# Performance work log

Hardware: AMD Instinct MI355X
Metric: run time of the kernel (lower is better)

Reference implementation:

```python
import jax, jax.numpy as jnp
import numpy as np
from jax import lax

B, T, A, L, H, FD = 32, 64, 6, 32, 128, 256


def setup_inputs() -> dict:
    key = jax.random.key(0)
    ks = jax.random.split(key, 24)
    rn = lambda k, s, sc: jax.random.normal(k, s, jnp.float32) * sc
    return {
        "states": rn(ks[0], (B, T, 3, 64, 64), 1.0),
        "actions": rn(ks[1], (B, T, A), 1.0),
        # CNN encoder params (scale ~ 1/sqrt(fan_in))
        "c1_w": rn(ks[2], (32, 3, 4, 4), 0.14), "c1_b": rn(ks[3], (32,), 0.01),
        "c2_w": rn(ks[4], (64, 32, 4, 4), 0.044), "c2_b": rn(ks[5], (64,), 0.01),
        "c3_w": rn(ks[6], (128, 64, 4, 4), 0.031), "c3_b": rn(ks[7], (128,), 0.01),
        "c4_w": rn(ks[8], (256, 128, 4, 4), 0.022), "c4_b": rn(ks[9], (256,), 0.01),
        "fc_w": rn(ks[10], (FD, 256 * 4 * 4), 0.0156), "fc_b": rn(ks[11], (FD,), 0.01),
        # GRUCell params (torch layout: W_ih (3H, in), W_hh (3H, H))
        "gru_wih": rn(ks[12], (3 * H, L + A), 0.16), "gru_whh": rn(ks[13], (3 * H, H), 0.088),
        "gru_bih": rn(ks[14], (3 * H,), 0.01), "gru_bhh": rn(ks[15], (3 * H,), 0.01),
        "prior_w": rn(ks[16], (2 * L, H), 0.088), "prior_b": rn(ks[17], (2 * L,), 0.01),
        "post_w": rn(ks[18], (2 * L, H + FD), 0.05), "post_b": rn(ks[19], (2 * L,), 0.01),
        # reparameterization noise (randn_like in torch), one per (b, t)
        "eps": rn(ks[20], (B, T, L), 1.0),
    }


def _conv(x, w, b):
    # Conv2d(k=4, stride=2, pad=1), NCHW/OIHW
    y = lax.conv_general_dilated(x, w, window_strides=(2, 2),
                                 padding=[(1, 1), (1, 1)],
                                 dimension_numbers=("NCHW", "OIHW", "NCHW"))
    return jax.nn.relu(y + b[None, :, None, None])


def _encode(x, c1_w, c1_b, c2_w, c2_b, c3_w, c3_b, c4_w, c4_b, fc_w, fc_b):
    # x: (N, 3, 64, 64) -> (N, FD)
    x = _conv(x, c1_w, c1_b)
    x = _conv(x, c2_w, c2_b)
    x = _conv(x, c3_w, c3_b)
    x = _conv(x, c4_w, c4_b)  # (N, 256, 4, 4)
    x = x.reshape(x.shape[0], -1)
    return x @ fc_w.T + fc_b


def _gru_cell(x, h, wih, whh, bih, bhh):
    gi = x @ wih.T + bih
    gh = h @ whh.T + bhh
    i_r, i_z, i_n = jnp.split(gi, 3, axis=-1)
    h_r, h_z, h_n = jnp.split(gh, 3, axis=-1)
    r = jax.nn.sigmoid(i_r + h_r)
    z = jax.nn.sigmoid(i_z + h_z)
    n = jnp.tanh(i_n + r * h_n)
    return (1.0 - z) * n + z * h


def reference(states, actions, c1_w, c1_b, c2_w, c2_b, c3_w, c3_b, c4_w, c4_b,
              fc_w, fc_b, gru_wih, gru_whh, gru_bih, gru_bhh,
              prior_w, prior_b, post_w, post_b, eps):
    b, t = states.shape[0], states.shape[1]
    # encoder has no recurrent dependency: encode all frames at once
    feats = _encode(states.reshape(b * t, *states.shape[2:]),
                    c1_w, c1_b, c2_w, c2_b, c3_w, c3_b, c4_w, c4_b,
                    fc_w, fc_b).reshape(b, t, -1)  # (B, T, FD)

    def step(carry, inp):
        h, z = carry
        a_t, f_t, e_t = inp
        h = _gru_cell(jnp.concatenate([z, a_t], -1), h,
                      gru_wih, gru_whh, gru_bih, gru_bhh)
        mu_p, lv_p = jnp.split(h @ prior_w.T + prior_b, 2, axis=-1)
        mu_q, lv_q = jnp.split(jnp.concatenate([h, f_t], -1) @ post_w.T + post_b, 2, axis=-1)
        z = mu_q + jnp.exp(0.5 * lv_q) * e_t
        return (h, z), (mu_p, lv_p, mu_q, lv_q, h, z)

    h0 = jnp.zeros((b, gru_whh.shape[1]), states.dtype)
    z0 = jnp.zeros((b, prior_w.shape[0] // 2), states.dtype)
    xs = (jnp.swapaxes(actions, 0, 1), jnp.swapaxes(feats, 0, 1),
          jnp.swapaxes(eps, 0, 1))
    _, ys = lax.scan(step, (h0, z0), xs)
    # (T, B, d) -> (B, T, d)
    return tuple(jnp.swapaxes(y, 0, 1) for y in ys)
```

## Files before the change

### kernel.cpp

```cpp
#include <hip/hip_runtime.h>
#include <math.h>

#define Bn 32
#define Tn 64
#define An 6
#define Ln 32
#define Hn 128
#define FDn 256
#define Nimg (Bn*Tn)

typedef __attribute__((ext_vector_type(8))) short frag_ab;
typedef __attribute__((ext_vector_type(4))) float frag_cd;
typedef _Float16 h2_t __attribute__((ext_vector_type(2)));

__device__ __forceinline__ float sigmoid_fast(float x){
  return __builtin_amdgcn_rcpf(1.f + __expf(-x));
}
__device__ __forceinline__ float tanh_fast(float x){
  float x2 = fminf(fmaxf(2.f*x, -30.f), 30.f);
  float e = __expf(x2);
  return (e - 1.f) * __builtin_amdgcn_rcpf(e + 1.f);
}

__device__ __forceinline__ unsigned short f2bf(float f){
  unsigned int u = __float_as_uint(f);
  unsigned int r = (u + 0x7fffu + ((u >> 16) & 1u)) >> 16;
  return (unsigned short)r;
}
__device__ __forceinline__ unsigned packh(float a, float b){
  union { h2_t h; unsigned u; } x;
  x.h = (h2_t){(_Float16)a, (_Float16)b};
  return x.u;
}
__device__ __forceinline__ float fdot2u(unsigned a, unsigned b, float c){
  union { unsigned u; h2_t h; } ua, ub;
  ua.u = a; ub.u = b;
#if __has_builtin(__builtin_amdgcn_fdot2)
  return __builtin_amdgcn_fdot2(ua.h, ub.h, c, false);
#else
  return c + (float)ua.h.x*(float)ub.h.x + (float)ua.h.y*(float)ub.h.y;
#endif
}
#define BAR_LDS() asm volatile("s_waitcnt lgkmcnt(0)\n\ts_barrier" ::: "memory")

__device__ __forceinline__ int swz_w(int r, int p){
  return ((r >> 4) << 9) + (p << 7) + ((((r & 15) ^ (p << 2))) << 3);
}
__device__ __forceinline__ int swz_r(int f, int l){
  return (f << 9) + ((l >> 4) << 7) + ((((l & 15) ^ ((l >> 4) << 2))) << 3);
}

__global__ void __launch_bounds__(256)
states_nhwc_kernel(const float* __restrict__ src, unsigned short* __restrict__ dst)
{
  int idx = blockIdx.x*256 + threadIdx.x;
  int n = idx >> 12, pix = idx & 4095;
  const float* s = src + (size_t)n*3*4096 + pix;
  union { unsigned short e[4]; uint2 v; } u;
  u.e[0] = f2bf(s[0]); u.e[1] = f2bf(s[4096]); u.e[2] = f2bf(s[8192]); u.e[3] = 0;
  *(uint2*)(dst + (size_t)idx*4) = u.v;
}

#define WHH4_U 24576
#define PO4_U  (64*53*4)
#define SCAN_U (WHH4_U + PO4_U)

__global__ void __launch_bounds__(256)
prep2_kernel(const float* __restrict__ c1w, const float* __restrict__ c2w,
             const float* __restrict__ c3w, const float* __restrict__ c4w,
             const float* __restrict__ fcw,
             const float* __restrict__ gwhh, const float* __restrict__ gwih,
             const float* __restrict__ prw,  const float* __restrict__ pow_,
             unsigned short* __restrict__ w1p, unsigned short* __restrict__ w2p,
             unsigned short* __restrict__ w3p, unsigned short* __restrict__ w4p,
             unsigned short* __restrict__ wfcp,
             unsigned* __restrict__ g_scan, unsigned* __restrict__ g_wih2,
             unsigned* __restrict__ g_pr2)
{
  const int bid = blockIdx.x, tid = threadIdx.x;
  if (bid < 128){
    int idx = bid*256+tid;
    int k = idx >> 9, r = idx & 511, tap = r >> 5, c = r & 31;
    w2p[idx] = f2bf(c2w[k*512 + c*16 + tap]);
  } else if (bid < 640){
    int idx = (bid-128)*256+tid;
    int k = idx >> 10, r = idx & 1023, tap = r >> 6, c = r & 63;
    w3p[idx] = f2bf(c3w[k*1024 + c*16 + tap]);
  } else if (bid < 2688){
    int idx = (bid-640)*256+tid;
    int k = idx >> 11, r = idx & 2047, tap = r >> 7, c = r & 127;
    w4p[idx] = f2bf(c4w[k*2048 + c*16 + tap]);
  } else if (bid < 6784){
    int idx = (bid-2688)*256+tid;
    int o = idx >> 12, r = idx & 4095, sp = r >> 8, c = r & 255;
    wfcp[idx] = f2bf(fcw[o*4096 + c*16 + sp]);
  } else if (bid < 6792){
    int idx = (bid-6784)*256+tid;
    int k = idx >> 6, r = idx & 63, tap = r >> 2, c = r & 3;
    w1p[idx] = (c < 3) ? f2bf(c1w[k*48 + c*16 + tap]) : (unsigned short)0;
  } else if (bid < 6888){
    int idx = (bid-6792)*256+tid;
    int q = idx & 3, r2 = idx >> 2;
    int k8 = r2 / 384, i = r2 - k8*384;
    int k = 8*k8 + 2*q;
    g_scan[idx] = packh(gwhh[i*128 + k], gwhh[i*128 + k + 1]);
  } else if (bid < 6917){
    int idx = (bid-6888)*256+tid;
    if (idx < 19*384){
      int c = idx / 384, i = idx - c*384;
      g_wih2[idx] = packh(gwih[i*38 + 2*c], gwih[i*38 + 2*c + 1]);
    }
  } else if (bid < 6933){
    int idx = (bid-6917)*256+tid;
    int o = idx >> 6, c = idx & 63;
    g_pr2[idx] = packh(prw[o*128 + 2*c], prw[o*128 + 2*c + 1]);
  } else {
    int idx = (bid-6933)*256+tid;
    if (idx < 64*192){
      int o = idx / 192, r2 = idx - o*192;
      int u = r2 >> 2, q = r2 & 3;
      int j = u / 12, kk = u - j*12;
      int k = 96*j + 8*kk + 2*q;
      g_scan[WHH4_U + (o*53 + j*13 + kk)*4 + q] =
        packh(pow_[o*384 + k], pow_[o*384 + k + 1]);
    }
  }
}

template<int Cin, int IN, int Kout, int OUT, int BN, int LOG_SPB>
__global__ void __launch_bounds__(256)
convN_mfma(const unsigned short* __restrict__ in,
           const unsigned short* __restrict__ wB,
           const float* __restrict__ bias,
           unsigned short* __restrict__ out)
{
  constexpr int SPB = OUT*OUT;
  constexpr int KD  = 16*Cin;
  constexpr int NCH = KD/32;
  constexpr int NFN = BN/32;
  constexpr int BFR = BN/16;
  __shared__ __align__(16) unsigned short Alds[2][8*512];
  __shared__ __align__(16) unsigned short Blds[2][BFR*512];

  const int tid = threadIdx.x;
  const int wave = tid >> 6, lane = tid & 63;
  const unsigned m0 = blockIdx.x * 128;
  const int n0 = blockIdx.y * BN;

  const int p = tid & 3;
  const unsigned short* baseA[2]; int oyA[2], oxA[2]; int AdstI[2];
#pragma unroll
  for (int h = 0; h < 2; h++){
    int r = (tid >> 2) + h*64;
    unsigned m = m0 + r;
    int nimg = m >> LOG_SPB;
    int sp = m & (SPB - 1);
    oyA[h] = sp / OUT; oxA[h] = sp & (OUT - 1);
    baseA[h] = in + (size_t)nimg * IN * IN * Cin;
    AdstI[h] = swz_w(r, p);
  }

  const int bn = tid >> 2, pb = tid & 3;
  const bool bAct = tid < BN*4;
  const unsigned short* Bsrc0 = wB + (size_t)(n0 + bn)*KD + pb*8;
  const int BdstI = swz_w(bn, pb);

  const int mhalf = wave >> 1, nhalf = wave & 1;
  frag_cd acc[4][NFN];
#pragma unroll
  for (int i = 0; i < 4; i++)
#pragma unroll
    for (int j = 0; j < NFN; j++) acc[i][j] = (frag_cd){0.f,0.f,0.f,0.f};

  auto loadA = [&](int kt, int h) -> uint4 {
    if constexpr (Cin >= 32){
      constexpr int CPT = Cin/32;
      int tap = kt / CPT;
      int c0 = (kt - tap*CPT)*32;
      int kh = tap >> 2, kw = tap & 3;
      int iy = 2*oyA[h] - 1 + kh;
      int ix = 2*oxA[h] - 1 + kw;
      uint4 v = {0u,0u,0u,0u};
      if ((unsigned)iy < (unsigned)IN && (unsigned)ix < (unsigned)IN)
        v = *(const uint4*)(baseA[h] + ((iy*IN + ix)*Cin + c0 + p*8));
      return v;
    } else {
      int kh = kt*2 + (p >> 1);
      int kw0 = (p & 1)*2;
      int iy = 2*oyA[h] - 1 + kh;
      int ix0 = 2*oxA[h] - 1 + kw0;
      union { uint2 u2[2]; uint4 u4; } v; v.u4 = (uint4){0u,0u,0u,0u};
      bool iyok = (unsigned)iy < (unsigned)IN;
      const unsigned short* rowp = baseA[h] + iy*IN*4;
#pragma unroll
      for (int d = 0; d < 2; d++){
        int ix = ix0 + d;
        if (iyok && (unsigned)ix < (unsigned)IN) v.u2[d] = *(const uint2*)(rowp + ix*4);
      }
      return v.u4;
    }
  };

  const int rdoff = swz_r(0, lane);

  uint4 aR0 = loadA(0,0), aR1 = loadA(0,1);
  uint4 bR = bAct ? *(const uint4*)Bsrc0 : (uint4){0u,0u,0u,0u};
  *(uint4*)&Alds[0][AdstI[0]] = aR0;
  *(uint4*)&Alds[0][AdstI[1]] = aR1;
  if (bAct) *(uint4*)&Blds[0][BdstI] = bR;
  if (NCH > 1){
    aR0 = loadA(1,0); aR1 = loadA(1,1);
    if (bAct) bR = *(const uint4*)(Bsrc0 + 32);
  }
  BAR_LDS();

#pragma unroll 2
  for (int kt = 0; kt < NCH; kt++){
    const int cur = kt & 1, nxt = cur ^ 1;
    if (kt + 1 < NCH){
      *(uint4*)&Alds[nxt][AdstI[0]] = aR0;
      *(uint4*)&Alds[nxt][AdstI[1]] = aR1;
      if (bAct) *(uint4*)&Blds[nxt][BdstI] = bR;
      if (kt + 2 < NCH){
        aR0 = loadA(kt+2, 0);
        aR1 = loadA(kt+2, 1);
        if (bAct) bR = *(const uint4*)(Bsrc0 + (kt+2)*32);
      }
    }
    frag_ab a[4], bf[NFN];
#pragma unroll
    for (int i = 0; i < 4; i++)
      a[i] = *(const frag_ab*)&Alds[cur][(((mhalf<<2) + i) << 9) + rdoff];
#pragma unroll
    for (int j = 0; j < NFN; j++)
      bf[j] = *(const frag_ab*)&Blds[cur][((nhalf*NFN + j) << 9) + rdoff];
#pragma unroll
    for (int i = 0; i < 4; i++)
#pragma unroll
      for (int j = 0; j < NFN; j++)
        acc[i][j] = __builtin_amdgcn_mfma_f32_16x16x32_bf16(a[i], bf[j], acc[i][j], 0, 0, 0);
    BAR_LDS();
  }

  const unsigned mb = m0 + mhalf*64 + ((lane >> 4) << 2);
#pragma unroll
  for (int j = 0; j < NFN; j++){
    const int kg = n0 + nhalf*(NFN*16) + j*16 + (lane & 15);
    const float bv = bias[kg];
#pragma unroll
    for (int i = 0; i < 4; i++){
#pragma unroll
      for (int r = 0; r < 4; r++){
        unsigned mg = mb + i*16 + r;
        out[(size_t)mg*Kout + kg] = f2bf(fmaxf(acc[i][j][r] + bv, 0.f));
      }
    }
  }
}

__global__ void __launch_bounds__(256)
fc_mfma2(const unsigned short* __restrict__ A, const unsigned short* __restrict__ wB,
         const float* __restrict__ bias, float* __restrict__ outF)
{
  constexpr int KD = 4096, NCH = KD/32;
  __shared__ __align__(16) unsigned short Alds[2][4*512];
  __shared__ __align__(16) unsigned short Blds[2][4*512];

  const int tid = threadIdx.x, wave = tid >> 6, lane = tid & 63;
  const int m0 = blockIdx.x * 64, n0 = blockIdx.y * 64;
  const int r = tid >> 2, pc = tid & 3;
  const unsigned short* Asrc = A + (size_t)(m0 + r)*KD + pc*8;
  const unsigned short* Bsrc = wB + (size_t)(n0 + r)*KD + pc*8;
  const int wI = swz_w(r, pc);
  const int mh = wave >> 1, nh = wave & 1;
  const int rdoff = swz_r(0, lane);

  frag_cd acc[2][2];
#pragma unroll
  for (int i = 0; i < 2; i++)
#pragma unroll
    for (int j = 0; j < 2; j++) acc[i][j] = (frag_cd){0.f,0.f,0.f,0.f};

  uint4 aP = *(const uint4*)Asrc, bP = *(const uint4*)Bsrc;
  *(uint4*)&Alds[0][wI] = aP;
  *(uint4*)&Blds[0][wI] = bP;
  aP = *(const uint4*)(Asrc + 32);
  bP = *(const uint4*)(Bsrc + 32);
  BAR_LDS();

#pragma unroll 2
  for (int kt = 0; kt < NCH; kt++){
    const int cur = kt & 1, nxt = cur ^ 1;
    if (kt + 1 < NCH){
      *(uint4*)&Alds[nxt][wI] = aP;
      *(uint4*)&Blds[nxt][wI] = bP;
      if (kt + 2 < NCH){
        aP = *(const uint4*)(Asrc + (kt+2)*32);
        bP = *(const uint4*)(Bsrc + (kt+2)*32);
      }
    }
    frag_ab a[2], b[2];
#pragma unroll
    for (int i = 0; i < 2; i++) a[i] = *(const frag_ab*)&Alds[cur][(((mh<<1)+i) << 9) + rdoff];
#pragma unroll
    for (int j = 0; j < 2; j++) b[j] = *(const frag_ab*)&Blds[cur][(((nh<<1)+j) << 9) + rdoff];
#pragma unroll
    for (int i = 0; i < 2; i++)
#pragma unroll
      for (int j = 0; j < 2; j++)
        acc[i][j] = __builtin_amdgcn_mfma_f32_16x16x32_bf16(a[i], b[j], acc[i][j], 0, 0, 0);
    BAR_LDS();
  }

  const int mb = m0 + mh*32 + ((lane >> 4) << 2);
#pragma unroll
  for (int j = 0; j < 2; j++){
    const int kg = n0 + nh*32 + j*16 + (lane & 15);
    const float bv = bias[kg];
#pragma unroll
    for (int i = 0; i < 2; i++)
#pragma unroll
      for (int rr = 0; rr < 4; rr++)
        outF[(size_t)(mb + i*16 + rr)*256 + kg] = acc[i][j][rr] + bv;
  }
}

__global__ void __launch_bounds__(384)
rssm_scan4(const float* __restrict__ actions, const float* __restrict__ feats,
           const float* __restrict__ eps,
           const unsigned* __restrict__ g_scan,
           const unsigned* __restrict__ g_wih2,
           const unsigned* __restrict__ g_pr2,
           const float* __restrict__ bih,  const float* __restrict__ bhh,
           const float* __restrict__ prior_b, const float* __restrict__ post_b,
           float* __restrict__ out)
{
  __shared__ __align__(16) _Float16 sh_hfh[384];
  __shared__ __align__(16) _Float16 sh_xh[40];
  __shared__ __align__(16) float sh_gi[384];
  __shared__ __align__(16) float sh_gh[384];

  const int b = blockIdx.x, tid = threadIdx.x;

  uint4 whhr[16];
  {
    const uint4* src = (const uint4*)g_scan;
#pragma unroll
    for (int k8 = 0; k8 < 16; k8++) whhr[k8] = src[k8*384 + tid];
  }
  unsigned wih[19];
#pragma unroll
  for (int c = 0; c < 19; c++) wih[c] = g_wih2[c*384 + tid];

  unsigned prw[32];
  float prb = 0.f;
  if (tid < 128){
    const unsigned* src = g_pr2 + (tid >> 1)*64 + (tid & 1)*32;
#pragma unroll
    for (int c = 0; c < 32; c++) prw[c] = src[c];
    prb = prior_b[tid >> 1];
  }

  int om = 0, pj = 0, o_p = 0; bool is_mu = false; float pob = 0.f;
  uint4 pww[12];
  if (tid >= 128){
    const int tt = tid - 128;
    om = tt >> 2; pj = tt & 3;
    o_p = (om >> 1) + (om & 1)*32;
    is_mu = !(om & 1);
    pob = post_b[o_p];
    const uint4* src = (const uint4*)(g_scan + WHH4_U) + o_p*53 + pj*13;
#pragma unroll
    for (int kk = 0; kk < 12; kk++) pww[kk] = src[kk];
  }

  const float bih_i = bih[tid], bhh_i = bhh[tid];
  float hreg = 0.f;

  {
    const int bt0 = b*Tn;
    if (tid < Hn) sh_hfh[tid] = (_Float16)0.f;
    if (tid < Ln) sh_xh[tid] = (_Float16)0.f;
    if (tid >= 32 && tid < 38) sh_xh[tid] = (_Float16)actions[(size_t)bt0*An + (tid-32)];
    if (tid >= 64 && tid < 320) sh_hfh[128 + tid - 64] = (_Float16)feats[(size_t)bt0*FDn + (tid-64)];
  }
  __syncthreads();

  const uint4* H4   = (const uint4*)sh_hfh;
  const unsigned* X2 = (const unsigned*)sh_xh;

  const int OFF_MUP = 0;
  const int OFF_LVP = Bn*Tn*Ln;
  const int OFF_MUQ = 2*Bn*Tn*Ln;
  const int OFF_LVQ = 3*Bn*Tn*Ln;
  const int OFF_H   = 4*Bn*Tn*Ln;
  const int OFF_Z   = 4*Bn*Tn*Ln + Bn*Tn*Hn;

  float freg = 0.f, areg = 0.f, epsr = 0.f;

  for (int t = 0; t < Tn; t++){
    const int bt = b*Tn + t;

    if (t > 0 && tid >= 64 && tid < 320) sh_hfh[128 + tid - 64] = (_Float16)freg;
    if (t < Tn-1){
      if (tid >= 64 && tid < 320) freg = feats[(size_t)(bt+1)*FDn + (tid-64)];
      if (tid >= 320 && tid < 326) areg = actions[(size_t)(bt+1)*An + (tid-320)];
    }
    if (tid >= 128 && ((tid-128)&7) == 0) epsr = eps[(size_t)bt*Ln + ((tid-128)>>3)];

    {
      float a0 = bih_i, a1 = 0.f;
#pragma unroll
      for (int c = 0; c < 19; c += 2) a0 = fdot2u(wih[c], X2[c], a0);
#pragma unroll
      for (int c = 1; c < 19; c += 2) a1 = fdot2u(wih[c], X2[c], a1);
      sh_gi[tid] = a0 + a1;

      float g0 = bhh_i, g1 = 0.f, g2 = 0.f, g3 = 0.f;
#pragma unroll
      for (int k8 = 0; k8 < 16; k8++){
        uint4 w = whhr[k8];
        uint4 h = H4[k8];
        g0 = fdot2u(w.x, h.x, g0);
        g1 = fdot2u(w.y, h.y, g1);
        g2 = fdot2u(w.z, h.z, g2);
        g3 = fdot2u(w.w, h.w, g3);
      }
      sh_gh[tid] = (g0 + g1) + (g2 + g3);
    }
    BAR_LDS();

    if (tid < Hn){
      const float r  = sigmoid_fast(sh_gi[tid]       + sh_gh[tid]);
      const float zg = sigmoid_fast(sh_gi[Hn  + tid] + sh_gh[Hn  + tid]);
      const float nn = tanh_fast(fmaf(r, sh_gh[2*Hn + tid], sh_gi[2*Hn + tid]));
      hreg = (1.f - zg)*nn + zg*hreg;
      sh_hfh[tid] = (_Float16)hreg;
      out[OFF_H + (size_t)bt*Hn + tid] = hreg;
    }
    if (t < Tn-1 && tid >= 320 && tid < 326) sh_xh[32 + tid - 320] = (_Float16)areg;
    BAR_LDS();

    if (tid < 128){
      const int j = tid & 1;
      float a0 = 0.f, a1 = 0.f, a2 = 0.f, a3 = 0.f;
#pragma unroll
      for (int c4 = 0; c4 < 8; c4++){
        uint4 h = H4[8*j + c4];
        a0 = fdot2u(prw[4*c4+0], h.x, a0);
        a1 = fdot2u(prw[4*c4+1], h.y, a1);
        a2 = fdot2u(prw[4*c4+2], h.z, a2);
        a3 = fdot2u(prw[4*c4+3], h.w, a3);
      }
      float p = (a0 + a1) + (a2 + a3);
      p += __shfl_xor(p, 1);
      if (j == 0){
        const int o = tid >> 1;
        p += prb;
        if (o < Ln) out[OFF_MUP + (size_t)bt*Ln + o] = p;
        else        out[OFF_LVP + (size_t)bt*Ln + (o - Ln)] = p;
      }
    } else {
      float a0 = 0.f, a1 = 0.f, a2 = 0.f, a3 = 0.f;
#pragma unroll
      for (int kk = 0; kk < 12; kk++){
        uint4 w = pww[kk];
        uint4 h = H4[pj*12 + kk];
        a0 = fdot2u(w.x, h.x, a0);
        a1 = fdot2u(w.y, h.y, a1);
        a2 = fdot2u(w.z, h.z, a2);
        a3 = fdot2u(w.w, h.w, a3);
      }
      float p = (a0 + a1) + (a2 + a3);
      p += __shfl_xor(p, 1);
      p += __shfl_xor(p, 2);
      p += pob;
      const float q_part = __shfl_xor(p, 4);
      if (pj == 0){
        if (is_mu){
          const int o = om >> 1;
          out[OFF_MUQ + (size_t)bt*Ln + o] = p;
          const float zz = fmaf(__expf(0.5f*q_part), epsr, p);
          sh_xh[o] = (_Float16)zz;
          out[OFF_Z + (size_t)bt*Ln + o] = zz;
        } else {
          out[OFF_LVQ + (size_t)bt*Ln + (o_p - Ln)] = p;
        }
      }
    }
    BAR_LDS();
  }
}

extern "C" void kernel_launch(void* const* d_in, const int* in_sizes, int n_in,
                              void* d_out, int out_size, void* d_ws, size_t ws_size,
                              hipStream_t stream)
{
  const float* states = (const float*)d_in[0];
  const float* actions= (const float*)d_in[1];
  const float* c1_w = (const float*)d_in[2];  const float* c1_b = (const float*)d_in[3];
  const float* c2_w = (const float*)d_in[4];  const float* c2_b = (const float*)d_in[5];
  const float* c3_w = (const float*)d_in[6];  const float* c3_b = (const float*)d_in[7];
  const float* c4_w = (const float*)d_in[8];  const float* c4_b = (const float*)d_in[9];
  const float* fc_w = (const float*)d_in[10]; const float* fc_b = (const float*)d_in[11];
  const float* gwih = (const float*)d_in[12]; const float* gwhh = (const float*)d_in[13];
  const float* gbih = (const float*)d_in[14]; const float* gbhh = (const float*)d_in[15];
  const float* pr_w = (const float*)d_in[16]; const float* pr_b = (const float*)d_in[17];
  const float* po_w = (const float*)d_in[18]; const float* po_b = (const float*)d_in[19];
  const float* eps  = (const float*)d_in[20];

  char* p = (char*)d_ws;
  auto alloc = [&](size_t bytes){ char* r = p; p += (bytes + 255) & ~255ULL; return r; };

  unsigned short* statesB = (unsigned short*)alloc((size_t)Nimg*4096*4*2);
  unsigned short* act1    = (unsigned short*)alloc((size_t)Nimg*1024*32*2);
  unsigned short* act2    = (unsigned short*)alloc((size_t)Nimg*256*64*2);
  unsigned short* act3    = (unsigned short*)alloc((size_t)Nimg*64*128*2);
  unsigned short* act4    = (unsigned short*)alloc((size_t)Nimg*16*256*2);
  float*          feats   = (float*)alloc((size_t)Nimg*FDn*4);
  unsigned short* w1p     = (unsigned short*)alloc(32*64*2);
  unsigned short* w2p     = (unsigned short*)alloc((size_t)64*512*2);
  unsigned short* w3p     = (unsigned short*)alloc((size_t)128*1024*2);
  unsigned short* w4p     = (unsigned short*)alloc((size_t)256*2048*2);
  unsigned short* wfcp    = (unsigned short*)alloc((size_t)256*4096*2);
  unsigned* g_scan = (unsigned*)alloc((size_t)SCAN_U*4);
  unsigned* g_wih2 = (unsigned*)alloc((size_t)19*384*4);
  unsigned* g_pr2  = (unsigned*)alloc((size_t)64*64*4);

  states_nhwc_kernel<<<Nimg*4096/256, 256, 0, stream>>>(states, statesB);
  prep2_kernel<<<6981, 256, 0, stream>>>(c1_w, c2_w, c3_w, c4_w, fc_w,
                                         gwhh, gwih, pr_w, po_w,
                                         w1p, w2p, w3p, w4p, wfcp,
                                         g_scan, g_wih2, g_pr2);

  convN_mfma<4,64,32,32,32,10>  <<< dim3(Nimg*1024/128, 1), 256, 0, stream >>>(statesB, w1p, c1_b, act1);
  convN_mfma<32,32,64,16,64,8>  <<< dim3(Nimg*256/128, 1), 256, 0, stream >>>(act1, w2p, c2_b, act2);
  convN_mfma<64,16,128,8,64,6>  <<< dim3(Nimg*64/128, 2), 256, 0, stream >>>(act2, w3p, c3_b, act3);
  convN_mfma<128,8,256,4,64,4>  <<< dim3(Nimg*16/128, 4), 256, 0, stream >>>(act3, w4p, c4_b, act4);

  fc_mfma2<<< dim3(Nimg/64, 4), 256, 0, stream >>>(act4, wfcp, fc_b, feats);

  rssm_scan4<<< Bn, 384, 0, stream >>>(actions, feats, eps,
                                       g_scan, g_wih2, g_pr2,
                                       gbih, gbhh, pr_b, po_b, (float*)d_out);
}
```

Before: 621.4 us.

## Pre-swizzle weights into MFMA fragment layout and load B directly to registers

The weight-prep kernel now writes conv and FC weights in a fragment-major layout, so each lane can load its MFMA B operand straight from global memory into registers. This removes the B staging through LDS and its swizzle. The wave tiling changes so each wave covers 32 rows by the full N tile, and the FC kernel gets a narrower N tile with twice the grid in y. The cost is more global and L2 weight traffic per wave and more B registers held for double buffering.

Measured after the change: 640.4 us. 3.1% more time.

```diff
diff --git a/kernel.cpp b/kernel.cpp
--- a/kernel.cpp
+++ b/kernel.cpp
@@ -43,12 +43,13 @@
 }
 #define BAR_LDS() asm volatile("s_waitcnt lgkmcnt(0)\n\ts_barrier" ::: "memory")
 
-__device__ __forceinline__ int swz_w(int r, int p){
-  return ((r >> 4) << 9) + (p << 7) + ((((r & 15) ^ (p << 2))) << 3);
-}
-__device__ __forceinline__ int swz_r(int f, int l){
-  return (f << 9) + ((l >> 4) << 7) + ((((l & 15) ^ ((l >> 4) << 2))) << 3);
-}
+__device__ __forceinline__ int aswz_w(int r, int p){
+  return ((r >> 4) << 9) + (p << 7) + (((r & 15) ^ (p << 1)) << 3);
+}
+__device__ __forceinline__ int aswz_r(int lane){
+  return ((lane >> 4) << 7) + (((lane & 15) ^ ((lane >> 4) << 1)) << 3);
+}
+
 
 __global__ void __launch_bounds__(256)
 states_nhwc_kernel(const float* __restrict__ src, unsigned short* __restrict__ dst)
@@ -80,24 +81,36 @@
   const int bid = blockIdx.x, tid = threadIdx.x;
   if (bid < 128){
     int idx = bid*256+tid;
-    int k = idx >> 9, r = idx & 511, tap = r >> 5, c = r & 31;
-    w2p[idx] = f2bf(c2w[k*512 + c*16 + tap]);
+    int k = idx >> 9, kd = idx & 511;
+    int tap = kd >> 5, c = kd & 31;
+    int dst = ((kd>>5)*4 + (k>>4))*512 + ((((kd>>3)&3)<<4) + (k&15))*8 + (kd&7);
+    w2p[dst] = f2bf(c2w[k*512 + c*16 + tap]);
   } else if (bid < 640){
     int idx = (bid-128)*256+tid;
-    int k = idx >> 10, r = idx & 1023, tap = r >> 6, c = r & 63;
-    w3p[idx] = f2bf(c3w[k*1024 + c*16 + tap]);
+    int k = idx >> 10, kd = idx & 1023;
+    int tap = kd >> 6, c = kd & 63;
+    int dst = ((kd>>5)*8 + (k>>4))*512 + ((((kd>>3)&3)<<4) + (k&15))*8 + (kd&7);
+    w3p[dst] = f2bf(c3w[k*1024 + c*16 + tap]);
   } else if (bid < 2688){
     int idx = (bid-640)*256+tid;
-    int k = idx >> 11, r = idx & 2047, tap = r >> 7, c = r & 127;
-    w4p[idx] = f2bf(c4w[k*2048 + c*16 + tap]);
+    int k = idx >> 11, kd = idx & 2047;
+    int tap = kd >> 7, c = kd & 127;
+    int dst = ((kd>>5)*16 + (k>>4))*512 + ((((kd>>3)&3)<<4) + (k&15))*8 + (kd&7);
+    w4p[dst] = f2bf(c4w[k*2048 + c*16 + tap]);
   } else if (bid < 6784){
     int idx = (bid-2688)*256+tid;
-    int o = idx >> 12, r = idx & 4095, sp = r >> 8, c = r & 255;
-    wfcp[idx] = f2bf(fcw[o*4096 + c*16 + sp]);
+    int k = idx >> 12, kd = idx & 4095;
+    int sp = kd >> 8, c = kd & 255;
+    int dst = ((kd>>5)*16 + (k>>4))*512 + ((((kd>>3)&3)<<4) + (k&15))*8 + (kd&7);
+    wfcp[dst] = f2bf(fcw[k*4096 + c*16 + sp]);
   } else if (bid < 6792){
     int idx = (bid-6784)*256+tid;
-    int k = idx >> 6, r = idx & 63, tap = r >> 2, c = r & 3;
-    w1p[idx] = (c < 3) ? f2bf(c1w[k*48 + c*16 + tap]) : (unsigned short)0;
+    if (idx < 2048){
+      int k = idx >> 6, kd = idx & 63;
+      int tap = kd >> 2, c = kd & 3;
+      int dst = ((kd>>5)*2 + (k>>4))*512 + ((((kd>>3)&3)<<4) + (k&15))*8 + (kd&7);
+      w1p[dst] = (c < 3) ? f2bf(c1w[k*48 + c*16 + tap]) : (unsigned short)0;
+    }
   } else if (bid < 6888){
     int idx = (bid-6792)*256+tid;
     int q = idx & 3, r2 = idx >> 2;
@@ -130,22 +143,21 @@
 template<int Cin, int IN, int Kout, int OUT, int BN, int LOG_SPB>
 __global__ void __launch_bounds__(256)
 convN_mfma(const unsigned short* __restrict__ in,
-           const unsigned short* __restrict__ wB,
+           const unsigned short* __restrict__ wB2,
            const float* __restrict__ bias,
            unsigned short* __restrict__ out)
 {
   constexpr int SPB = OUT*OUT;
   constexpr int KD  = 16*Cin;
   constexpr int NCH = KD/32;
-  constexpr int NFN = BN/32;
-  constexpr int BFR = BN/16;
+  constexpr int NFN = BN/16;
+  constexpr int KF  = Kout/16;
   __shared__ __align__(16) unsigned short Alds[2][8*512];
-  __shared__ __align__(16) unsigned short Blds[2][BFR*512];
 
   const int tid = threadIdx.x;
   const int wave = tid >> 6, lane = tid & 63;
   const unsigned m0 = blockIdx.x * 128;
-  const int n0 = blockIdx.y * BN;
+  const int nf0 = blockIdx.y * NFN;
 
   const int p = tid & 3;
   const unsigned short* baseA[2]; int oyA[2], oxA[2]; int AdstI[2];
@@ -157,18 +169,15 @@
     int sp = m & (SPB - 1);
     oyA[h] = sp / OUT; oxA[h] = sp & (OUT - 1);
     baseA[h] = in + (size_t)nimg * IN * IN * Cin;
-    AdstI[h] = swz_w(r, p);
-  }
-
-  const int bn = tid >> 2, pb = tid & 3;
-  const bool bAct = tid < BN*4;
-  const unsigned short* Bsrc0 = wB + (size_t)(n0 + bn)*KD + pb*8;
-  const int BdstI = swz_w(bn, pb);
-
-  const int mhalf = wave >> 1, nhalf = wave & 1;
-  frag_cd acc[4][NFN];
-#pragma unroll
-  for (int i = 0; i < 4; i++)
+    AdstI[h] = aswz_w(r, p);
+  }
+
+  const unsigned short* wBl = wB2 + (size_t)nf0*512 + lane*8;
+  const int rdoff = aswz_r(lane);
+
+  frag_cd acc[2][NFN];
+#pragma unroll
+  for (int i = 0; i < 2; i++)
 #pragma unroll
     for (int j = 0; j < NFN; j++) acc[i][j] = (frag_cd){0.f,0.f,0.f,0.f};
 
@@ -201,17 +210,19 @@
     }
   };
 
-  const int rdoff = swz_r(0, lane);
+  union U4F { uint4 u; frag_ab f; };
+  U4F bR[2][NFN];
 
   uint4 aR0 = loadA(0,0), aR1 = loadA(0,1);
-  uint4 bR = bAct ? *(const uint4*)Bsrc0 : (uint4){0u,0u,0u,0u};
+#pragma unroll
+  for (int j = 0; j < NFN; j++) bR[0][j].u = *(const uint4*)(wBl + j*512);
+  if (NCH > 1){
+#pragma unroll
+    for (int j = 0; j < NFN; j++) bR[1][j].u = *(const uint4*)(wBl + (KF + j)*512);
+  }
   *(uint4*)&Alds[0][AdstI[0]] = aR0;
   *(uint4*)&Alds[0][AdstI[1]] = aR1;
-  if (bAct) *(uint4*)&Blds[0][BdstI] = bR;
-  if (NCH > 1){
-    aR0 = loadA(1,0); aR1 = loadA(1,1);
-    if (bAct) bR = *(const uint4*)(Bsrc0 + 32);
-  }
+  if (NCH > 1){ aR0 = loadA(1,0); aR1 = loadA(1,1); }
   BAR_LDS();
 
 #pragma unroll 2
@@ -220,72 +231,71 @@
     if (kt + 1 < NCH){
       *(uint4*)&Alds[nxt][AdstI[0]] = aR0;
       *(uint4*)&Alds[nxt][AdstI[1]] = aR1;
-      if (bAct) *(uint4*)&Blds[nxt][BdstI] = bR;
-      if (kt + 2 < NCH){
-        aR0 = loadA(kt+2, 0);
-        aR1 = loadA(kt+2, 1);
-        if (bAct) bR = *(const uint4*)(Bsrc0 + (kt+2)*32);
-      }
-    }
-    frag_ab a[4], bf[NFN];
-#pragma unroll
-    for (int i = 0; i < 4; i++)
-      a[i] = *(const frag_ab*)&Alds[cur][(((mhalf<<2) + i) << 9) + rdoff];
-#pragma unroll
-    for (int j = 0; j < NFN; j++)
-      bf[j] = *(const frag_ab*)&Blds[cur][((nhalf*NFN + j) << 9) + rdoff];
-#pragma unroll
-    for (int i = 0; i < 4; i++)
+      if (kt + 2 < NCH){ aR0 = loadA(kt+2, 0); aR1 = loadA(kt+2, 1); }
+    }
+    frag_ab a[2];
+#pragma unroll
+    for (int i = 0; i < 2; i++)
+      a[i] = *(const frag_ab*)&Alds[cur][(((wave<<1) + i) << 9) + rdoff];
+#pragma unroll
+    for (int i = 0; i < 2; i++)
 #pragma unroll
       for (int j = 0; j < NFN; j++)
-        acc[i][j] = __builtin_amdgcn_mfma_f32_16x16x32_bf16(a[i], bf[j], acc[i][j], 0, 0, 0);
+        acc[i][j] = __builtin_amdgcn_mfma_f32_16x16x32_bf16(a[i], bR[cur][j].f, acc[i][j], 0, 0, 0);
+    if (kt + 2 < NCH){
+#pragma unroll
+      for (int j = 0; j < NFN; j++)
+        bR[cur][j].u = *(const uint4*)(wBl + ((size_t)(kt+2)*KF + j)*512);
+    }
     BAR_LDS();
   }
 
-  const unsigned mb = m0 + mhalf*64 + ((lane >> 4) << 2);
+  const unsigned mbW = m0 + wave*32 + ((lane >> 4) << 2);
 #pragma unroll
   for (int j = 0; j < NFN; j++){
-    const int kg = n0 + nhalf*(NFN*16) + j*16 + (lane & 15);
+    const int kg = (nf0 + j)*16 + (lane & 15);
     const float bv = bias[kg];
 #pragma unroll
-    for (int i = 0; i < 4; i++){
-#pragma unroll
-      for (int r = 0; r < 4; r++){
-        unsigned mg = mb + i*16 + r;
-        out[(size_t)mg*Kout + kg] = f2bf(fmaxf(acc[i][j][r] + bv, 0.f));
+    for (int i = 0; i < 2; i++){
+#pragma unroll
+      for (int r4 = 0; r4 < 4; r4++){
+        unsigned mg = mbW + i*16 + r4;
+        out[(size_t)mg*Kout + kg] = f2bf(fmaxf(acc[i][j][r4] + bv, 0.f));
       }
     }
   }
 }
 
 __global__ void __launch_bounds__(256)
-fc_mfma2(const unsigned short* __restrict__ A, const unsigned short* __restrict__ wB,
+fc_mfma3(const unsigned short* __restrict__ A, const unsigned short* __restrict__ wB2,
          const float* __restrict__ bias, float* __restrict__ outF)
 {
-  constexpr int KD = 4096, NCH = KD/32;
+  constexpr int KD = 4096, NCH = KD/32, KF = 16, NFN = 2;
   __shared__ __align__(16) unsigned short Alds[2][4*512];
-  __shared__ __align__(16) unsigned short Blds[2][4*512];
 
   const int tid = threadIdx.x, wave = tid >> 6, lane = tid & 63;
-  const int m0 = blockIdx.x * 64, n0 = blockIdx.y * 64;
+  const int m0 = blockIdx.x * 64;
+  const int nf0 = blockIdx.y * NFN;
   const int r = tid >> 2, pc = tid & 3;
   const unsigned short* Asrc = A + (size_t)(m0 + r)*KD + pc*8;
-  const unsigned short* Bsrc = wB + (size_t)(n0 + r)*KD + pc*8;
-  const int wI = swz_w(r, pc);
-  const int mh = wave >> 1, nh = wave & 1;
-  const int rdoff = swz_r(0, lane);
-
-  frag_cd acc[2][2];
-#pragma unroll
-  for (int i = 0; i < 2; i++)
-#pragma unroll
-    for (int j = 0; j < 2; j++) acc[i][j] = (frag_cd){0.f,0.f,0.f,0.f};
-
-  uint4 aP = *(const uint4*)Asrc, bP = *(const uint4*)Bsrc;
+  const int wI = aswz_w(r, pc);
+  const unsigned short* wBl = wB2 + (size_t)nf0*512 + lane*8;
+  const int rdoff = aswz_r(lane);
+
+  frag_cd acc[NFN];
+#pragma unroll
+  for (int j = 0; j < NFN; j++) acc[j] = (frag_cd){0.f,0.f,0.f,0.f};
+
+  union U4F { uint4 u; frag_ab f; };
+  U4F bR[2][NFN];
+
+  uint4 aP = *(const uint4*)Asrc;
+#pragma unroll
+  for (int j = 0; j < NFN; j++) bR[0][j].u = *(const uint4*)(wBl + j*512);
+#pragma unroll
+  for (int j = 0; j < NFN; j++) bR[1][j].u = *(const uint4*)(wBl + (KF + j)*512);
   *(uint4*)&Alds[0][wI] = aP;
-  *(uint4*)&Blds[0][wI] = bP;
   aP = *(const uint4*)(Asrc + 32);
-  bP = *(const uint4*)(Bsrc + 32);
   BAR_LDS();
 
 #pragma unroll 2
@@ -293,35 +303,28 @@
     const int cur = kt & 1, nxt = cur ^ 1;
     if (kt + 1 < NCH){
       *(uint4*)&Alds[nxt][wI] = aP;
-      *(uint4*)&Blds[nxt][wI] = bP;
-      if (kt + 2 < NCH){
-        aP = *(const uint4*)(Asrc + (kt+2)*32);
-        bP = *(const uint4*)(Bsrc + (kt+2)*32);
-      }
-    }
-    frag_ab a[2], b[2];
-#pragma unroll
-    for (int i = 0; i < 2; i++) a[i] = *(const frag_ab*)&Alds[cur][(((mh<<1)+i) << 9) + rdoff];
-#pragma unroll
-    for (int j = 0; j < 2; j++) b[j] = *(const frag_ab*)&Blds[cur][(((nh<<1)+j) << 9) + rdoff];
-#pragma unroll
-    for (int i = 0; i < 2; i++)
-#pragma unroll
-      for (int j = 0; j < 2; j++)
-        acc[i][j] = __builtin_amdgcn_mfma_f32_16x16x32_bf16(a[i], b[j], acc[i][j], 0, 0, 0);
+      if (kt + 2 < NCH) aP = *(const uint4*)(Asrc + (kt+2)*32);
+    }
+    frag_ab a = *(const frag_ab*)&Alds[cur][(wave << 9) + rdoff];
+#pragma unroll
+    for (int j = 0; j < NFN; j++)
+      acc[j] = __builtin_amdgcn_mfma_f32_16x16x32_bf16(a, bR[cur][j].f, acc[j], 0, 0, 0);
+    if (kt + 2 < NCH){
+#pragma unroll
+      for (int j = 0; j < NFN; j++)
+        bR[cur][j].u = *(const uint4*)(wBl + ((size_t)(kt+2)*KF + j)*512);
+    }
     BAR_LDS();
   }
 
-  const int mb = m0 + mh*32 + ((lane >> 4) << 2);
-#pragma unroll
-  for (int j = 0; j < 2; j++){
-    const int kg = n0 + nh*32 + j*16 + (lane & 15);
+  const int mb = m0 + wave*16 + ((lane >> 4) << 2);
+#pragma unroll
+  for (int j = 0; j < NFN; j++){
+    const int kg = (nf0 + j)*16 + (lane & 15);
     const float bv = bias[kg];
 #pragma unroll
-    for (int i = 0; i < 2; i++)
-#pragma unroll
-      for (int rr = 0; rr < 4; rr++)
-        outF[(size_t)(mb + i*16 + rr)*256 + kg] = acc[i][j][rr] + bv;
+    for (int r4 = 0; r4 < 4; r4++)
+      outF[(size_t)(mb + r4)*256 + kg] = acc[j][r4] + bv;
   }
 }
 
@@ -538,7 +541,7 @@
   convN_mfma<64,16,128,8,64,6>  <<< dim3(Nimg*64/128, 2), 256, 0, stream >>>(act2, w3p, c3_b, act3);
   convN_mfma<128,8,256,4,64,4>  <<< dim3(Nimg*16/128, 4), 256, 0, stream >>>(act3, w4p, c4_b, act4);
 
-  fc_mfma2<<< dim3(Nimg/64, 4), 256, 0, stream >>>(act4, wfcp, fc_b, feats);
+  fc_mfma3<<< dim3(Nimg/64, 8), 256, 0, stream >>>(act4, wfcp, fc_b, feats);
 
   rssm_scan4<<< Bn, 384, 0, stream >>>(actions, feats, eps,
                                        g_scan, g_wih2, g_pr2,
```
